# Kernel optimization log

Hardware: AMD Instinct MI355X
Metric: run time of the kernel (lower is better)

The kernel has to match this reference:

```python
import jax, jax.numpy as jnp
import numpy as np

B, T, D, H = 4, 2048, 768, 12
HD = D // H  # 64


def setup_inputs() -> dict:
    key = jax.random.key(0)
    ks = jax.random.split(key, 6)
    s = 0.02
    return {
        "x": jax.random.normal(ks[0], (B, T, D), dtype=jnp.float32),
        "Wq": jax.random.normal(ks[1], (D, D), dtype=jnp.float32) * s,
        "Wk": jax.random.normal(ks[2], (D, D), dtype=jnp.float32) * s,
        "Wv": jax.random.normal(ks[3], (D, D), dtype=jnp.float32) * s,
        "Wo": jax.random.normal(ks[4], (D, D), dtype=jnp.float32) * s,
        "bo": jnp.zeros((D,), dtype=jnp.float32),
    }


def reference(x, Wq, Wk, Wv, Wo, bo):
    b, t, d = x.shape
    # projections (torch Linear: y = x @ W.T; here W stored as [d_in, d_out])
    q = (x @ Wq).reshape(b, t, H, HD).transpose(0, 2, 1, 3)  # [b,H,T,hd]
    k = (x @ Wk).reshape(b, t, H, HD).transpose(0, 2, 1, 3)
    v = (x @ Wv).reshape(b, t, H, HD).transpose(0, 2, 1, 3)
    scores = jnp.einsum("bhqd,bhkd->bhqk", q, k)  # [b,H,T,T]
    causal = jnp.tril(jnp.ones((t, t), dtype=bool))  # True = keep
    scores = jnp.where(causal, scores, -jnp.inf)
    w = jax.nn.softmax(scores / jnp.sqrt(jnp.asarray(HD, scores.dtype)), axis=-1)
    # dropout p=0.0 (eval) -> identity
    ctx = jnp.einsum("bhqk,bhkd->bqhd", w, v).reshape(b, t, d)
    return ctx @ Wo + bo
```

## Files before the change

kernel.cpp:

```cpp
#include <hip/hip_runtime.h>
#include <cstdint>
#include <cstddef>

typedef unsigned short u16;
typedef __attribute__((ext_vector_type(8))) short short8;
typedef __attribute__((ext_vector_type(4))) short short4v;
typedef __attribute__((ext_vector_type(4))) float floatx4;
typedef __attribute__((ext_vector_type(8))) unsigned short ushortx8;
typedef __attribute__((ext_vector_type(4))) unsigned short ushortx4;

__device__ __forceinline__ u16 f2b(float f) {
    unsigned u = __float_as_uint(f);
    u += 0x7fffu + ((u >> 16) & 1u);
    return (u16)(u >> 16);
}
__device__ __forceinline__ float b2f(u16 b) {
    return __uint_as_float(((unsigned)b) << 16);
}
__device__ __forceinline__ float ex2(float x) {
    return __builtin_amdgcn_exp2f(x);
}
__device__ __forceinline__ unsigned pk2(float a, float b) {
    return __builtin_amdgcn_perm(__float_as_uint(b), __float_as_uint(a),
                                 0x07060302u);
}
__device__ __forceinline__ short4v pack4(float a, float b, float c, float d) {
    unsigned long long q =
        ((unsigned long long)pk2(c, d) << 32) | (unsigned long long)pk2(a, b);
    return __builtin_bit_cast(short4v, q);
}

#define MFMA16(a, b, c) __builtin_amdgcn_mfma_f32_16x16x16bf16_1k(a, b, c, 0, 0, 0)
#define MFMA32(a, b, c) __builtin_amdgcn_mfma_f32_16x16x32_bf16(a, b, c, 0, 0, 0)

#define QSCALE 0.18033688011112042f

__global__ __launch_bounds__(256) void cvt_x_kernel(const float* __restrict__ x,
                                                    u16* __restrict__ xb, int n4) {
    int i = blockIdx.x * 256 + threadIdx.x;
    if (i >= n4) return;
    float4 v = ((const float4*)x)[i];
    ushortx4 u;
    u.x = f2b(v.x); u.y = f2b(v.y); u.z = f2b(v.z); u.w = f2b(v.w);
    ((ushortx4*)xb)[i] = u;
}

__global__ __launch_bounds__(256) void cvt_wT_kernel(
    const float* __restrict__ W0, const float* __restrict__ W1,
    const float* __restrict__ W2, const float* __restrict__ W3,
    u16* __restrict__ o0, u16* __restrict__ o1,
    u16* __restrict__ o2, u16* __restrict__ o3) {
    const float* W = (blockIdx.z == 0) ? W0 : (blockIdx.z == 1) ? W1
                     : (blockIdx.z == 2) ? W2 : W3;
    u16* O = (blockIdx.z == 0) ? o0 : (blockIdx.z == 1) ? o1
             : (blockIdx.z == 2) ? o2 : o3;
    __shared__ float tile[32][33];
    int n0 = blockIdx.x * 32, k0 = blockIdx.y * 32;
    int tx = threadIdx.x & 31;
    int ty = threadIdx.x >> 5;
#pragma unroll
    for (int j = 0; j < 32; j += 8)
        tile[ty + j][tx] = W[(size_t)(k0 + ty + j) * 768 + n0 + tx];
    __syncthreads();
#pragma unroll
    for (int j = 0; j < 32; j += 8)
        O[(size_t)(n0 + ty + j) * 768 + k0 + tx] = f2b(tile[tx][ty + j]);
}

__global__ __launch_bounds__(256) void gemm_qkv_kernel(
    const u16* __restrict__ A,
    const u16* __restrict__ Bt0, const u16* __restrict__ Bt1,
    const u16* __restrict__ Bt2,
    u16* __restrict__ O0, u16* __restrict__ O1, u16* __restrict__ O2) {
    constexpr int Kd = 768;
    const u16* Bt = (blockIdx.z == 0) ? Bt0 : (blockIdx.z == 1) ? Bt1 : Bt2;
    u16* Ob = (blockIdx.z == 0) ? O0 : (blockIdx.z == 1) ? O1 : O2;
    const bool vtrans = (blockIdx.z == 2);
    const float oscale = (blockIdx.z == 0) ? QSCALE : 1.0f;

    __shared__ u16 As[128 * 40];
    __shared__ u16 Bs[128 * 40];

    const int m0 = blockIdx.y * 128, n0 = blockIdx.x * 128;
    const int tid = threadIdx.x;
    const int lane = tid & 63, wave = tid >> 6;
    const int moff = (wave >> 1) * 64, noff = (wave & 1) * 64;
    const int lrow = lane & 15, lquad = lane >> 4;

    floatx4 acc[4][4] = {};

    const int sr = tid >> 2;
    const int sc = (tid & 3) * 8;
    const u16* Ap0 = A + (size_t)(m0 + sr) * Kd + sc;
    const u16* Ap1 = A + (size_t)(m0 + sr + 64) * Kd + sc;
    const u16* Bp0 = Bt + (size_t)(n0 + sr) * Kd + sc;
    const u16* Bp1 = Bt + (size_t)(n0 + sr + 64) * Kd + sc;
    u16* Asw0 = &As[sr * 40 + sc];
    u16* Asw1 = &As[(sr + 64) * 40 + sc];
    u16* Bsw0 = &Bs[sr * 40 + sc];
    u16* Bsw1 = &Bs[(sr + 64) * 40 + sc];
    const u16* Afr = &As[(moff + lrow) * 40 + lquad * 8];
    const u16* Bfr = &Bs[(noff + lrow) * 40 + lquad * 8];

    for (int k0 = 0; k0 < Kd; k0 += 32) {
        ushortx8 va0 = *(const ushortx8*)(Ap0 + k0);
        ushortx8 va1 = *(const ushortx8*)(Ap1 + k0);
        ushortx8 vb0 = *(const ushortx8*)(Bp0 + k0);
        ushortx8 vb1 = *(const ushortx8*)(Bp1 + k0);
        *(ushortx8*)Asw0 = va0;
        *(ushortx8*)Asw1 = va1;
        *(ushortx8*)Bsw0 = vb0;
        *(ushortx8*)Bsw1 = vb1;
        __syncthreads();
        short8 af[4], bf[4];
#pragma unroll
        for (int i = 0; i < 4; ++i) af[i] = *(const short8*)(Afr + i * 16 * 40);
#pragma unroll
        for (int j = 0; j < 4; ++j) bf[j] = *(const short8*)(Bfr + j * 16 * 40);
#pragma unroll
        for (int i = 0; i < 4; ++i)
#pragma unroll
            for (int j = 0; j < 4; ++j)
                acc[i][j] = MFMA32(af[i], bf[j], acc[i][j]);
        __syncthreads();
    }

    if (vtrans) {
#pragma unroll
        for (int i = 0; i < 4; ++i) {
            int gm = m0 + moff + i * 16 + lquad * 4;
            int bb = gm >> 11, t = gm & 2047;
#pragma unroll
            for (int j = 0; j < 4; ++j) {
                int gn = n0 + noff + j * 16 + lrow;
                int hh = gn >> 6, hd = gn & 63;
                ushortx4 w;
                w.x = f2b(acc[i][j][0]);
                w.y = f2b(acc[i][j][1]);
                w.z = f2b(acc[i][j][2]);
                w.w = f2b(acc[i][j][3]);
                *(ushortx4*)(Ob + (((size_t)(bb * 12 + hh) * 64 + hd) * 2048 + t)) = w;
            }
        }
    } else {
#pragma unroll
        for (int i = 0; i < 4; ++i) {
#pragma unroll
            for (int r = 0; r < 4; ++r) {
                int gm = m0 + moff + i * 16 + lquad * 4 + r;
                int bb = gm >> 11, t = gm & 2047;
#pragma unroll
                for (int j = 0; j < 4; ++j) {
                    int gn = n0 + noff + j * 16 + lrow;
                    float v = acc[i][j][r] * oscale;
                    int hh = gn >> 6, hd = gn & 63;
                    Ob[((size_t)(bb * 12 + hh) * 2048 + t) * 64 + hd] = f2b(v);
                }
            }
        }
    }
}

__global__ __launch_bounds__(256) void gemm_out_kernel(
    const u16* __restrict__ A, const u16* __restrict__ Bt,
    float* __restrict__ outf, const float* __restrict__ bias) {
    constexpr int Kd = 768;
    constexpr int Nd = 768;
    __shared__ u16 As[128 * 40];
    __shared__ u16 Bs[64 * 40];

    const int m0 = blockIdx.y * 128, n0 = blockIdx.x * 64;
    const int tid = threadIdx.x;
    const int lane = tid & 63, wave = tid >> 6;
    const int moff = (wave >> 1) * 64, noff = (wave & 1) * 32;
    const int lrow = lane & 15, lquad = lane >> 4;

    floatx4 acc[4][2] = {};

    const int sr = tid >> 2;
    const int sc = (tid & 3) * 8;
    const u16* Ap0 = A + (size_t)(m0 + sr) * Kd + sc;
    const u16* Ap1 = A + (size_t)(m0 + sr + 64) * Kd + sc;
    const u16* Bp0 = Bt + (size_t)(n0 + sr) * Kd + sc;
    u16* Asw0 = &As[sr * 40 + sc];
    u16* Asw1 = &As[(sr + 64) * 40 + sc];
    u16* Bsw0 = &Bs[sr * 40 + sc];
    const u16* Afr = &As[(moff + lrow) * 40 + lquad * 8];
    const u16* Bfr = &Bs[(noff + lrow) * 40 + lquad * 8];

    for (int k0 = 0; k0 < Kd; k0 += 32) {
        ushortx8 va0 = *(const ushortx8*)(Ap0 + k0);
        ushortx8 va1 = *(const ushortx8*)(Ap1 + k0);
        ushortx8 vb0 = *(const ushortx8*)(Bp0 + k0);
        *(ushortx8*)Asw0 = va0;
        *(ushortx8*)Asw1 = va1;
        *(ushortx8*)Bsw0 = vb0;
        __syncthreads();
        short8 af[4], bf[2];
#pragma unroll
        for (int i = 0; i < 4; ++i) af[i] = *(const short8*)(Afr + i * 16 * 40);
#pragma unroll
        for (int j = 0; j < 2; ++j) bf[j] = *(const short8*)(Bfr + j * 16 * 40);
#pragma unroll
        for (int i = 0; i < 4; ++i)
#pragma unroll
            for (int j = 0; j < 2; ++j)
                acc[i][j] = MFMA32(af[i], bf[j], acc[i][j]);
        __syncthreads();
    }

#pragma unroll
    for (int i = 0; i < 4; ++i) {
#pragma unroll
        for (int r = 0; r < 4; ++r) {
            int gm = m0 + moff + i * 16 + lquad * 4 + r;
#pragma unroll
            for (int j = 0; j < 2; ++j) {
                int gn = n0 + noff + j * 16 + lrow;
                outf[(size_t)gm * Nd + gn] = acc[i][j][r] + bias[gn];
            }
        }
    }
}

template <bool DIAG>
__device__ __forceinline__ void make_p(
    const floatx4 st[4], short4v p4[4], float& l,
    int wave, int lrow, int quad) {
#pragma unroll
    for (int jt = 0; jt < 4; ++jt) {
        if (DIAG && jt > wave) {
            p4[jt] = (short4v)0;
            continue;
        }
        float p[4];
#pragma unroll
        for (int r = 0; r < 4; ++r) {
            float e = ex2(st[jt][r]);
            if (DIAG && jt == wave && (quad * 4 + r) > lrow) e = 0.0f;
            p[r] = e;
            l += e;
        }
        p4[jt] = pack4(p[0], p[1], p[2], p[3]);
    }
}

__global__ __launch_bounds__(256, 3) void flash_attn_kernel(
    const u16* __restrict__ Qg, const u16* __restrict__ Kg,
    const u16* __restrict__ Vtg, u16* __restrict__ ctx) {
    const int bh = blockIdx.y;
    const int qa = blockIdx.x;
    const int qb = 31 - qa;
    const size_t base = (size_t)bh * 2048 * 64;

    __shared__ u16 Ks[2][64][72];
    __shared__ u16 Vts[2][64][72];

    const int tid = threadIdx.x;
    const int wave = tid >> 6, lane = tid & 63;
    const int lrow = lane & 15, quad = lane >> 4;
    const int lr = tid >> 2, ls = (tid & 3) * 16;
    const int q0[2] = {qa * 64, qb * 64};

    short8 qf[2][2];
#pragma unroll
    for (int s = 0; s < 2; ++s) {
        const u16* qsrc = Qg + base + (size_t)(q0[s] + wave * 16 + lrow) * 64 + quad * 8;
        qf[s][0] = *(const short8*)qsrc;
        qf[s][1] = *(const short8*)(qsrc + 32);
    }

    float l[2] = {0.f, 0.f};
    floatx4 o[2][4] = {};

    const u16* kp = Kg + base + (size_t)lr * 64 + ls;
    const u16* vp = Vtg + base + (size_t)lr * 2048 + ls;
    ushortx8 kr0 = *(const ushortx8*)kp;
    ushortx8 kr1 = *(const ushortx8*)(kp + 8);
    ushortx8 vr0 = *(const ushortx8*)vp;
    ushortx8 vr1 = *(const ushortx8*)(vp + 8);

    for (int kt = 0; kt <= qb; ++kt) {
        const int buf = kt & 1;
        *(ushortx8*)&Ks[buf][lr][ls] = kr0;
        *(ushortx8*)&Ks[buf][lr][ls + 8] = kr1;
        *(ushortx8*)&Vts[buf][lr][ls] = vr0;
        *(ushortx8*)&Vts[buf][lr][ls + 8] = vr1;
        if (kt < qb) {
            kp += 4096;
            vp += 64;
            kr0 = *(const ushortx8*)kp;
            kr1 = *(const ushortx8*)(kp + 8);
            vr0 = *(const ushortx8*)vp;
            vr1 = *(const ushortx8*)(vp + 8);
        }
        __syncthreads();

        const bool actA = (kt <= qa);

        floatx4 st0[4] = {}, st1[4] = {};
#pragma unroll
        for (int ks = 0; ks < 2; ++ks) {
#pragma unroll
            for (int jt = 0; jt < 4; ++jt) {
                short8 kf = *(const short8*)&Ks[buf][jt * 16 + lrow][ks * 32 + quad * 8];
                st1[jt] = MFMA32(kf, qf[1][ks], st1[jt]);
                if (actA) st0[jt] = MFMA32(kf, qf[0][ks], st0[jt]);
            }
        }

        short4v p40[4], p41[4];
        if (kt == qb) make_p<true>(st1, p41, l[1], wave, lrow, quad);
        else          make_p<false>(st1, p41, l[1], wave, lrow, quad);
        if (actA) {
            if (kt == qa) make_p<true>(st0, p40, l[0], wave, lrow, quad);
            else          make_p<false>(st0, p40, l[0], wave, lrow, quad);
        }

#pragma unroll
        for (int jt = 0; jt < 4; ++jt) {
            short4v vf[4];
#pragma unroll
            for (int dt = 0; dt < 4; ++dt)
                vf[dt] = *(const short4v*)&Vts[buf][dt * 16 + lrow][jt * 16 + quad * 4];
#pragma unroll
            for (int dt = 0; dt < 4; ++dt) {
                o[1][dt] = MFMA16(vf[dt], p41[jt], o[1][dt]);
                if (actA) o[0][dt] = MFMA16(vf[dt], p40[jt], o[0][dt]);
            }
        }
    }

    const int b = bh / 12, h = bh % 12;
#pragma unroll
    for (int s = 0; s < 2; ++s) {
        float lv = l[s];
        lv += __shfl_xor(lv, 16, 64);
        lv += __shfl_xor(lv, 32, 64);
        float inv = 1.0f / lv;
        int q = q0[s] + wave * 16 + lrow;
        u16* dst = ctx + ((size_t)(b * 2048 + q) * 12 + h) * 64 + quad * 4;
#pragma unroll
        for (int dt = 0; dt < 4; ++dt) {
            ushortx4 w;
            w.x = f2b(o[s][dt][0] * inv);
            w.y = f2b(o[s][dt][1] * inv);
            w.z = f2b(o[s][dt][2] * inv);
            w.w = f2b(o[s][dt][3] * inv);
            *(ushortx4*)(dst + dt * 16) = w;
        }
    }
}

extern "C" void kernel_launch(void* const* d_in, const int* in_sizes, int n_in,
                              void* d_out, int out_size, void* d_ws,
                              size_t ws_size, hipStream_t stream) {
    const float* x  = (const float*)d_in[0];
    const float* Wq = (const float*)d_in[1];
    const float* Wk = (const float*)d_in[2];
    const float* Wv = (const float*)d_in[3];
    const float* Wo = (const float*)d_in[4];
    const float* bo = (const float*)d_in[5];
    float* out = (float*)d_out;

    char* ws = (char*)d_ws;
    u16* xb   = (u16*)(ws);
    u16* wqb  = (u16*)(ws + 12582912);
    u16* wkb  = (u16*)(ws + 13762560);
    u16* wvb  = (u16*)(ws + 14942208);
    u16* wob  = (u16*)(ws + 16121856);
    u16* Qb   = (u16*)(ws + 17301504);
    u16* Kb   = (u16*)(ws + 29884416);
    u16* Vtb  = (u16*)(ws + 42467328);
    u16* ctxb = (u16*)(ws + 55050240);

    cvt_x_kernel<<<6144, 256, 0, stream>>>(x, xb, 8192 * 768 / 4);
    cvt_wT_kernel<<<dim3(24, 24, 4), 256, 0, stream>>>(Wq, Wk, Wv, Wo, wqb, wkb,
                                                       wvb, wob);
    gemm_qkv_kernel<<<dim3(6, 64, 3), 256, 0, stream>>>(
        xb, wqb, wkb, wvb, Qb, Kb, Vtb);
    flash_attn_kernel<<<dim3(16, 48), 256, 0, stream>>>(Qb, Kb, Vtb, ctxb);
    gemm_out_kernel<<<dim3(12, 64), 256, 0, stream>>>(ctxb, wob, out, bo);
}
```

Measured before the change: 223.6 us.

## Double-buffer GEMM tiles with async global-to-LDS loads and XCD-aware block mapping

Both projection GEMMs now stage A/B tiles with global_load_lds 16-byte direct-to-LDS copies into double-buffered, unpadded shared memory. The next tile is issued while MFMAs run on the current one, and the loop needs one barrier per step instead of two. Grids are flattened to 1D with a swizzle that spreads M tiles across the 8 XCDs for L2 locality. Launch bounds request 4 blocks per CU, including on flash attention. The risks are LDS bank conflicts from the unpadded 32-wide rows, uncertain vmcnt synchronization of the async copies, and register pressure from the tighter occupancy hint.

```diff
diff --git a/kernel.cpp b/kernel.cpp
--- a/kernel.cpp
+++ b/kernel.cpp
@@ -28,6 +28,12 @@
     unsigned long long q =
         ((unsigned long long)pk2(c, d) << 32) | (unsigned long long)pk2(a, b);
     return __builtin_bit_cast(short4v, q);
+}
+
+__device__ __forceinline__ void async_cp16(const void* g, void* l) {
+    __builtin_amdgcn_global_load_lds(
+        (const __attribute__((address_space(1))) unsigned int*)g,
+        (__attribute__((address_space(3))) unsigned int*)l, 16, 0, 0);
 }
 
 #define MFMA16(a, b, c) __builtin_amdgcn_mfma_f32_16x16x16bf16_1k(a, b, c, 0, 0, 0)
@@ -67,21 +73,27 @@
         O[(size_t)(n0 + ty + j) * 768 + k0 + tx] = f2b(tile[tx][ty + j]);
 }
 
-__global__ __launch_bounds__(256) void gemm_qkv_kernel(
+__global__ __launch_bounds__(256, 4) void gemm_qkv_kernel(
     const u16* __restrict__ A,
     const u16* __restrict__ Bt0, const u16* __restrict__ Bt1,
     const u16* __restrict__ Bt2,
     u16* __restrict__ O0, u16* __restrict__ O1, u16* __restrict__ O2) {
     constexpr int Kd = 768;
-    const u16* Bt = (blockIdx.z == 0) ? Bt0 : (blockIdx.z == 1) ? Bt1 : Bt2;
-    u16* Ob = (blockIdx.z == 0) ? O0 : (blockIdx.z == 1) ? O1 : O2;
-    const bool vtrans = (blockIdx.z == 2);
-    const float oscale = (blockIdx.z == 0) ? QSCALE : 1.0f;
-
-    __shared__ u16 As[128 * 40];
-    __shared__ u16 Bs[128 * 40];
-
-    const int m0 = blockIdx.y * 128, n0 = blockIdx.x * 128;
+    const int bid = blockIdx.x;
+    const int xcd = bid & 7, j = bid >> 3;
+    const int nIdx = j % 18;
+    const int mIdx = xcd + 8 * (j / 18);
+    const int z = nIdx / 6, nt = nIdx % 6;
+    const u16* Bt = (z == 0) ? Bt0 : (z == 1) ? Bt1 : Bt2;
+    u16* Ob = (z == 0) ? O0 : (z == 1) ? O1 : O2;
+    const bool vtrans = (z == 2);
+    const float oscale = (z == 0) ? QSCALE : 1.0f;
+
+    const int m0 = mIdx * 128, n0 = nt * 128;
+
+    __shared__ u16 As[2][128 * 32];
+    __shared__ u16 Bs[2][128 * 32];
+
     const int tid = threadIdx.x;
     const int lane = tid & 63, wave = tid >> 6;
     const int moff = (wave >> 1) * 64, noff = (wave & 1) * 64;
@@ -89,41 +101,36 @@
 
     floatx4 acc[4][4] = {};
 
-    const int sr = tid >> 2;
-    const int sc = (tid & 3) * 8;
-    const u16* Ap0 = A + (size_t)(m0 + sr) * Kd + sc;
-    const u16* Ap1 = A + (size_t)(m0 + sr + 64) * Kd + sc;
-    const u16* Bp0 = Bt + (size_t)(n0 + sr) * Kd + sc;
-    const u16* Bp1 = Bt + (size_t)(n0 + sr + 64) * Kd + sc;
-    u16* Asw0 = &As[sr * 40 + sc];
-    u16* Asw1 = &As[(sr + 64) * 40 + sc];
-    u16* Bsw0 = &Bs[sr * 40 + sc];
-    u16* Bsw1 = &Bs[(sr + 64) * 40 + sc];
-    const u16* Afr = &As[(moff + lrow) * 40 + lquad * 8];
-    const u16* Bfr = &Bs[(noff + lrow) * 40 + lquad * 8];
-
-    for (int k0 = 0; k0 < Kd; k0 += 32) {
-        ushortx8 va0 = *(const ushortx8*)(Ap0 + k0);
-        ushortx8 va1 = *(const ushortx8*)(Ap1 + k0);
-        ushortx8 vb0 = *(const ushortx8*)(Bp0 + k0);
-        ushortx8 vb1 = *(const ushortx8*)(Bp1 + k0);
-        *(ushortx8*)Asw0 = va0;
-        *(ushortx8*)Asw1 = va1;
-        *(ushortx8*)Bsw0 = vb0;
-        *(ushortx8*)Bsw1 = vb1;
+    const u16* Agp = A + (size_t)(m0 + wave * 32 + (lane >> 2)) * Kd + (lane & 3) * 8;
+    const u16* Bgp = Bt + (size_t)(n0 + wave * 32 + (lane >> 2)) * Kd + (lane & 3) * 8;
+
+#define QKV_ISSUE(buf, k0)                                              \
+    do {                                                                \
+        async_cp16(Agp + (k0), &As[buf][wave * 1024]);                  \
+        async_cp16(Agp + (k0) + 16 * Kd, &As[buf][wave * 1024 + 512]);  \
+        async_cp16(Bgp + (k0), &Bs[buf][wave * 1024]);                  \
+        async_cp16(Bgp + (k0) + 16 * Kd, &Bs[buf][wave * 1024 + 512]);  \
+    } while (0)
+
+    QKV_ISSUE(0, 0);
+    for (int kk = 0; kk < 24; ++kk) {
+        const int buf = kk & 1;
         __syncthreads();
         short8 af[4], bf[4];
 #pragma unroll
-        for (int i = 0; i < 4; ++i) af[i] = *(const short8*)(Afr + i * 16 * 40);
-#pragma unroll
-        for (int j = 0; j < 4; ++j) bf[j] = *(const short8*)(Bfr + j * 16 * 40);
-#pragma unroll
         for (int i = 0; i < 4; ++i)
-#pragma unroll
-            for (int j = 0; j < 4; ++j)
-                acc[i][j] = MFMA32(af[i], bf[j], acc[i][j]);
-        __syncthreads();
-    }
+            af[i] = *(const short8*)&As[buf][(moff + i * 16 + lrow) * 32 + lquad * 8];
+#pragma unroll
+        for (int jj = 0; jj < 4; ++jj)
+            bf[jj] = *(const short8*)&Bs[buf][(noff + jj * 16 + lrow) * 32 + lquad * 8];
+        if (kk < 23) QKV_ISSUE(buf ^ 1, (kk + 1) * 32);
+#pragma unroll
+        for (int i = 0; i < 4; ++i)
+#pragma unroll
+            for (int jj = 0; jj < 4; ++jj)
+                acc[i][jj] = MFMA32(af[i], bf[jj], acc[i][jj]);
+    }
+#undef QKV_ISSUE
 
     if (vtrans) {
 #pragma unroll
@@ -131,14 +138,14 @@
             int gm = m0 + moff + i * 16 + lquad * 4;
             int bb = gm >> 11, t = gm & 2047;
 #pragma unroll
-            for (int j = 0; j < 4; ++j) {
-                int gn = n0 + noff + j * 16 + lrow;
+            for (int jj = 0; jj < 4; ++jj) {
+                int gn = n0 + noff + jj * 16 + lrow;
                 int hh = gn >> 6, hd = gn & 63;
                 ushortx4 w;
-                w.x = f2b(acc[i][j][0]);
-                w.y = f2b(acc[i][j][1]);
-                w.z = f2b(acc[i][j][2]);
-                w.w = f2b(acc[i][j][3]);
+                w.x = f2b(acc[i][jj][0]);
+                w.y = f2b(acc[i][jj][1]);
+                w.z = f2b(acc[i][jj][2]);
+                w.w = f2b(acc[i][jj][3]);
                 *(ushortx4*)(Ob + (((size_t)(bb * 12 + hh) * 64 + hd) * 2048 + t)) = w;
             }
         }
@@ -150,9 +157,9 @@
                 int gm = m0 + moff + i * 16 + lquad * 4 + r;
                 int bb = gm >> 11, t = gm & 2047;
 #pragma unroll
-                for (int j = 0; j < 4; ++j) {
-                    int gn = n0 + noff + j * 16 + lrow;
-                    float v = acc[i][j][r] * oscale;
+                for (int jj = 0; jj < 4; ++jj) {
+                    int gn = n0 + noff + jj * 16 + lrow;
+                    float v = acc[i][jj][r] * oscale;
                     int hh = gn >> 6, hd = gn & 63;
                     Ob[((size_t)(bb * 12 + hh) * 2048 + t) * 64 + hd] = f2b(v);
                 }
@@ -161,15 +168,20 @@
     }
 }
 
-__global__ __launch_bounds__(256) void gemm_out_kernel(
+__global__ __launch_bounds__(256, 4) void gemm_out_kernel(
     const u16* __restrict__ A, const u16* __restrict__ Bt,
     float* __restrict__ outf, const float* __restrict__ bias) {
     constexpr int Kd = 768;
     constexpr int Nd = 768;
-    __shared__ u16 As[128 * 40];
-    __shared__ u16 Bs[64 * 40];
-
-    const int m0 = blockIdx.y * 128, n0 = blockIdx.x * 64;
+    const int bid = blockIdx.x;
+    const int xcd = bid & 7, j = bid >> 3;
+    const int nIdx = j % 12;
+    const int mIdx = xcd + 8 * (j / 12);
+    const int m0 = mIdx * 128, n0 = nIdx * 64;
+
+    __shared__ u16 As[2][128 * 32];
+    __shared__ u16 Bs[2][64 * 32];
+
     const int tid = threadIdx.x;
     const int lane = tid & 63, wave = tid >> 6;
     const int moff = (wave >> 1) * 64, noff = (wave & 1) * 32;
@@ -177,37 +189,35 @@
 
     floatx4 acc[4][2] = {};
 
-    const int sr = tid >> 2;
-    const int sc = (tid & 3) * 8;
-    const u16* Ap0 = A + (size_t)(m0 + sr) * Kd + sc;
-    const u16* Ap1 = A + (size_t)(m0 + sr + 64) * Kd + sc;
-    const u16* Bp0 = Bt + (size_t)(n0 + sr) * Kd + sc;
-    u16* Asw0 = &As[sr * 40 + sc];
-    u16* Asw1 = &As[(sr + 64) * 40 + sc];
-    u16* Bsw0 = &Bs[sr * 40 + sc];
-    const u16* Afr = &As[(moff + lrow) * 40 + lquad * 8];
-    const u16* Bfr = &Bs[(noff + lrow) * 40 + lquad * 8];
-
-    for (int k0 = 0; k0 < Kd; k0 += 32) {
-        ushortx8 va0 = *(const ushortx8*)(Ap0 + k0);
-        ushortx8 va1 = *(const ushortx8*)(Ap1 + k0);
-        ushortx8 vb0 = *(const ushortx8*)(Bp0 + k0);
-        *(ushortx8*)Asw0 = va0;
-        *(ushortx8*)Asw1 = va1;
-        *(ushortx8*)Bsw0 = vb0;
+    const u16* Agp = A + (size_t)(m0 + wave * 32 + (lane >> 2)) * Kd + (lane & 3) * 8;
+    const u16* Bgp = Bt + (size_t)(n0 + wave * 16 + (lane >> 2)) * Kd + (lane & 3) * 8;
+
+#define OUT_ISSUE(buf, k0)                                              \
+    do {                                                                \
+        async_cp16(Agp + (k0), &As[buf][wave * 1024]);                  \
+        async_cp16(Agp + (k0) + 16 * Kd, &As[buf][wave * 1024 + 512]);  \
+        async_cp16(Bgp + (k0), &Bs[buf][wave * 512]);                   \
+    } while (0)
+
+    OUT_ISSUE(0, 0);
+    for (int kk = 0; kk < 24; ++kk) {
+        const int buf = kk & 1;
         __syncthreads();
         short8 af[4], bf[2];
 #pragma unroll
-        for (int i = 0; i < 4; ++i) af[i] = *(const short8*)(Afr + i * 16 * 40);
-#pragma unroll
-        for (int j = 0; j < 2; ++j) bf[j] = *(const short8*)(Bfr + j * 16 * 40);
-#pragma unroll
         for (int i = 0; i < 4; ++i)
-#pragma unroll
-            for (int j = 0; j < 2; ++j)
-                acc[i][j] = MFMA32(af[i], bf[j], acc[i][j]);
-        __syncthreads();
-    }
+            af[i] = *(const short8*)&As[buf][(moff + i * 16 + lrow) * 32 + lquad * 8];
+#pragma unroll
+        for (int jj = 0; jj < 2; ++jj)
+            bf[jj] = *(const short8*)&Bs[buf][(noff + jj * 16 + lrow) * 32 + lquad * 8];
+        if (kk < 23) OUT_ISSUE(buf ^ 1, (kk + 1) * 32);
+#pragma unroll
+        for (int i = 0; i < 4; ++i)
+#pragma unroll
+            for (int jj = 0; jj < 2; ++jj)
+                acc[i][jj] = MFMA32(af[i], bf[jj], acc[i][jj]);
+    }
+#undef OUT_ISSUE
 
 #pragma unroll
     for (int i = 0; i < 4; ++i) {
@@ -215,9 +225,9 @@
         for (int r = 0; r < 4; ++r) {
             int gm = m0 + moff + i * 16 + lquad * 4 + r;
 #pragma unroll
-            for (int j = 0; j < 2; ++j) {
-                int gn = n0 + noff + j * 16 + lrow;
-                outf[(size_t)gm * Nd + gn] = acc[i][j][r] + bias[gn];
+            for (int jj = 0; jj < 2; ++jj) {
+                int gn = n0 + noff + jj * 16 + lrow;
+                outf[(size_t)gm * Nd + gn] = acc[i][jj][r] + bias[gn];
             }
         }
     }
@@ -245,7 +255,7 @@
     }
 }
 
-__global__ __launch_bounds__(256, 3) void flash_attn_kernel(
+__global__ __launch_bounds__(256, 4) void flash_attn_kernel(
     const u16* __restrict__ Qg, const u16* __restrict__ Kg,
     const u16* __restrict__ Vtg, u16* __restrict__ ctx) {
     const int bh = blockIdx.y;
@@ -377,8 +387,7 @@
     cvt_x_kernel<<<6144, 256, 0, stream>>>(x, xb, 8192 * 768 / 4);
     cvt_wT_kernel<<<dim3(24, 24, 4), 256, 0, stream>>>(Wq, Wk, Wv, Wo, wqb, wkb,
                                                        wvb, wob);
-    gemm_qkv_kernel<<<dim3(6, 64, 3), 256, 0, stream>>>(
-        xb, wqb, wkb, wvb, Qb, Kb, Vtb);
+    gemm_qkv_kernel<<<1152, 256, 0, stream>>>(xb, wqb, wkb, wvb, Qb, Kb, Vtb);
     flash_attn_kernel<<<dim3(16, 48), 256, 0, stream>>>(Qb, Kb, Vtb, ctxb);
-    gemm_out_kernel<<<dim3(12, 64), 256, 0, stream>>>(ctxb, wob, out, bo);
-}
+    gemm_out_kernel<<<768, 256, 0, stream>>>(ctxb, wob, out, bo);
+}
```

After: 290.4 us. 29.9% more time.
